# Kernel optimization log

Measured on AMD Instinct MI355X. Metric: run time of the kernel, lower is better.

## Reference

```python
import jax, jax.numpy as jnp
import numpy as np

B, L, D, H = 4, 1024, 512, 8
DH = D // H
NUM_BUCKETS = 8
MAX_DIST = 8
N_GAT_LAYERS = 2
NEG = jnp.finfo(jnp.float32).min


def _ln(x, g, b):
    m = x.mean(-1, keepdims=True)
    v = ((x - m) ** 2).mean(-1, keepdims=True)
    return (x - m) * jax.lax.rsqrt(v + 1e-5) * g + b


def _adj(parents):
    # undirected child<->parent adjacency, no self loops. parents: [B,L] int
    Bb, Ll = parents.shape
    valid = (parents >= 0) & (parents < Ll)
    p = jnp.clip(parents, 0, Ll - 1)
    bidx = jnp.arange(Bb)[:, None]
    cidx = jnp.arange(Ll)[None, :]
    A = jnp.zeros((Bb, Ll, Ll), jnp.int32).at[bidx, cidx, p].add(valid.astype(jnp.int32))
    return (A + A.transpose(0, 2, 1)) > 0


def _bucketized_dist(adj):
    # Bounded BFS: exact tree distances up to MAX_DIST; everything farther
    # lands in the same clamped bucket as distance MAX_DIST (faithful to
    # clamp(d, max=MAX_DIST) then clamp(max=NUM_BUCKETS-1) in the original).
    Bb, Ll, _ = adj.shape
    eye = jnp.eye(Ll, dtype=bool)
    Af = adj.astype(jnp.float32)
    reach = jnp.broadcast_to(eye, (Bb, Ll, Ll))
    dist = jnp.broadcast_to(jnp.where(eye, 0, MAX_DIST).astype(jnp.int32), (Bb, Ll, Ll))
    for s in range(1, MAX_DIST + 1):
        nxt = (jnp.matmul(reach.astype(jnp.float32), Af) > 0) | reach
        dist = jnp.where(nxt & ~reach, s, dist)
        reach = nxt
    return jnp.minimum(dist, NUM_BUCKETS - 1)  # bucket indices [B,L,L]


def _tree_bias(bias_table, parents, pad_mask):
    buckets = _bucketized_dist(_adj(parents))          # [B,L,L]
    bias = bias_table[:, buckets]                      # [H,B,L,L]
    bias = jnp.transpose(bias, (1, 0, 2, 3))           # [B,H,L,L]
    valid = pad_mask[:, None, None, :] & pad_mask[:, None, :, None]
    return jnp.where(valid, bias, NEG)


def _heads(z):
    Bb, Ll, _ = z.shape
    return jnp.transpose(z.reshape(Bb, Ll, H, DH), (0, 2, 1, 3))


def _attn(x, parents, pad_mask, ln1_g, ln1_b, qkv_w, qkv_b, out_w, out_b, bias_table):
    h = _ln(x, ln1_g, ln1_b)
    Bb, Ll, _ = h.shape
    qkv = (h @ qkv_w + qkv_b).reshape(Bb, Ll, 3, H, DH)
    q = jnp.transpose(qkv[:, :, 0], (0, 2, 1, 3))
    k = jnp.transpose(qkv[:, :, 1], (0, 2, 1, 3))
    v = jnp.transpose(qkv[:, :, 2], (0, 2, 1, 3))
    logits = jnp.einsum('bhid,bhjd->bhij', q, k) / np.float32(np.sqrt(DH))
    logits = logits + _tree_bias(bias_table, parents, pad_mask)
    logits = jnp.where(pad_mask[:, None, None, :], logits, NEG)
    a = jax.nn.softmax(logits, axis=-1)
    y = jnp.einsum('bhij,bhjd->bhid', a, v)
    y = jnp.transpose(y, (0, 2, 1, 3)).reshape(Bb, Ll, D)
    return y @ out_w + out_b


def _gat(x, adj_sl, pad_mask, ln_g, ln_b, wq_w, wq_b, wk_w, wk_b, wv_w, wv_b, out_w, out_b):
    h = _ln(x, ln_g, ln_b)
    Bb, Ll, _ = h.shape
    q, k, v = _heads(h @ wq_w + wq_b), _heads(h @ wk_w + wk_b), _heads(h @ wv_w + wv_b)
    logits = jnp.einsum('bhid,bhjd->bhij', q, k) / np.float32(np.sqrt(DH))
    logits = jnp.where(adj_sl[:, None], logits, NEG)
    logits = jnp.where(pad_mask[:, None, None, :], logits, NEG)
    a = jax.nn.softmax(logits, axis=-1)
    y = jnp.einsum('bhij,bhjd->bhid', a, v)
    y = jnp.transpose(y, (0, 2, 1, 3)).reshape(Bb, Ll, D)
    return x + (y @ out_w + out_b)


def _forward(x, parents, pad_mask, ln1_g, ln1_b, qkv_w, qkv_b, attn_out_w, attn_out_b,
             bias_table, gat_ln_g, gat_ln_b, gat_wq_w, gat_wq_b, gat_wk_w, gat_wk_b,
             gat_wv_w, gat_wv_b, gat_out_w, gat_out_b):
    x = x + _attn(x, parents, pad_mask, ln1_g, ln1_b, qkv_w, qkv_b,
                  attn_out_w, attn_out_b, bias_table)
    adj = _adj(parents)
    eye = jnp.eye(adj.shape[1], dtype=bool)
    adj_sl = (adj | eye) & pad_mask[:, :, None] & pad_mask[:, None, :]
    for l in range(N_GAT_LAYERS):
        x = _gat(x, adj_sl, pad_mask, gat_ln_g[l], gat_ln_b[l],
                 gat_wq_w[l], gat_wq_b[l], gat_wk_w[l], gat_wk_b[l],
                 gat_wv_w[l], gat_wv_b[l], gat_out_w[l], gat_out_b[l])
    return x


def setup_inputs() -> dict:
    key = jax.random.key(0)
    ks = jax.random.split(key, 16)
    x = jax.random.normal(ks[0], (B, L, D), jnp.float32)
    # valid random tree: parents[i] in [0, i-1], root (i=0) has parent -1
    u = jax.random.uniform(ks[1], (B, L))
    parents = jnp.floor(u * jnp.arange(L, dtype=jnp.float32)).astype(jnp.int32)
    parents = parents.at[:, 0].set(-1)
    pad_mask = jnp.ones((B, L), dtype=bool)
    w = lambda k, shp: jax.random.normal(k, shp, jnp.float32) * 0.02
    return {
        'x': x, 'parents': parents, 'pad_mask': pad_mask,
        'ln1_g': jnp.ones((D,), jnp.float32), 'ln1_b': jnp.zeros((D,), jnp.float32),
        'qkv_w': w(ks[2], (D, 3 * D)), 'qkv_b': jnp.zeros((3 * D,), jnp.float32),
        'attn_out_w': w(ks[3], (D, D)), 'attn_out_b': jnp.zeros((D,), jnp.float32),
        'bias_table': w(ks[4], (H, NUM_BUCKETS)),
        'gat_ln_g': jnp.ones((N_GAT_LAYERS, D), jnp.float32),
        'gat_ln_b': jnp.zeros((N_GAT_LAYERS, D), jnp.float32),
        'gat_wq_w': w(ks[5], (N_GAT_LAYERS, D, D)), 'gat_wq_b': jnp.zeros((N_GAT_LAYERS, D), jnp.float32),
        'gat_wk_w': w(ks[6], (N_GAT_LAYERS, D, D)), 'gat_wk_b': jnp.zeros((N_GAT_LAYERS, D), jnp.float32),
        'gat_wv_w': w(ks[7], (N_GAT_LAYERS, D, D)), 'gat_wv_b': jnp.zeros((N_GAT_LAYERS, D), jnp.float32),
        'gat_out_w': w(ks[8], (N_GAT_LAYERS, D, D)), 'gat_out_b': jnp.zeros((N_GAT_LAYERS, D), jnp.float32),
    }


def reference(x, parents, pad_mask, ln1_g, ln1_b, qkv_w, qkv_b, attn_out_w, attn_out_b,
              bias_table, gat_ln_g, gat_ln_b, gat_wq_w, gat_wq_b, gat_wk_w, gat_wk_b,
              gat_wv_w, gat_wv_b, gat_out_w, gat_out_b):
    return _forward(x, parents, pad_mask, ln1_g, ln1_b, qkv_w, qkv_b, attn_out_w,
                    attn_out_b, bias_table, gat_ln_g, gat_ln_b, gat_wq_w, gat_wq_b,
                    gat_wk_w, gat_wk_b, gat_wv_w, gat_wv_b, gat_out_w, gat_out_b)
```

## Files before the change

kernel.cpp:

```cpp
#include <hip/hip_runtime.h>
#include <hip/hip_bf16.h>
#include <math.h>

#define BB 4
#define LL 1024
#define DD 512
#define HH 8
#define DHH 64
#define MASKF -3.0e38f
#define FIXM 10.0f
#define NSPLIT 2

#define MODE_QKV 0
#define MODE_QKVR 1
#define MODE_F32C 2
#define MODE_F32S 3

typedef __attribute__((ext_vector_type(4))) float f32x4;
typedef __attribute__((ext_vector_type(8))) __bf16 bf16x8;

__device__ __forceinline__ unsigned short f2bf(float x) {
  return __builtin_bit_cast(unsigned short, __float2bfloat16(x));
}
__device__ __forceinline__ float bf2f(unsigned int u16) {
  unsigned int v = u16 << 16;
  return __builtin_bit_cast(float, v);
}
__device__ __forceinline__ float wave_sum(float v) {
#pragma unroll
  for (int o = 32; o > 0; o >>= 1) v += __shfl_xor(v, o, 64);
  return v;
}
__device__ __forceinline__ void gl16(const void* g, void* l) {
  __builtin_amdgcn_global_load_lds(
      (const __attribute__((address_space(1))) unsigned int*)g,
      (__attribute__((address_space(3))) unsigned int*)l, 16, 0, 0);
}

__global__ __launch_bounds__(256) void prep_kernel(
    const int* __restrict__ parents, const float* w0, const float* w1,
    const float* w2, const float* w3, const float* w4, const float* w5,
    const float* w6, const float* w7, const float* w8, const float* w9,
    unsigned char* __restrict__ bfr, unsigned short* __restrict__ wt) {
  __shared__ __align__(16) char psm[16640];
  const int bid = blockIdx.x;
  const int tid = threadIdx.x;
  if (bid < 1024) {
    int* si = reinterpret_cast<int*>(psm);
    int* sj = si + 576;
    const int jt = bid & 15, qt = (bid >> 4) & 15, b = bid >> 8;
    if (tid < 128) {
      const int* pp = parents + b * 1024;
      const int base = (tid < 64) ? (qt * 64 + tid) : (jt * 64 + (tid - 64));
      int* dst = (tid < 64) ? (si + tid * 9) : (sj + (tid - 64) * 9);
      int cur = base;
      dst[0] = cur;
#pragma unroll
      for (int s = 1; s <= 8; ++s) {
        int nxt = -1;
        if (cur >= 0) {
          int p = pp[cur];
          if (p >= 0 && p < 1024) nxt = p;
        }
        dst[s] = nxt;
        cur = nxt;
      }
    }
    __syncthreads();
    const int w = tid >> 6, lane = tid & 63, g = lane >> 4, lr = lane & 15;
    int ui[9];
#pragma unroll
    for (int a = 0; a < 9; ++a) ui[a] = si[(w * 16 + lr) * 9 + a];
    unsigned int dw[4];
#pragma unroll
    for (int t = 0; t < 4; ++t) {
      unsigned int d = 0;
#pragma unroll
      for (int r = 0; r < 4; ++r) {
        const int jl = t * 16 + g * 4 + r;
        int uj[9];
#pragma unroll
        for (int c = 0; c < 9; ++c) uj[c] = sj[jl * 9 + c];
        int dist = 255;
#pragma unroll
        for (int a = 0; a < 9; ++a) {
          const int va = ui[a];
          if (va >= 0) {
#pragma unroll
            for (int c = 0; c < 9; ++c)
              if (va == uj[c] && a + c < dist) dist = a + c;
          }
        }
        d |= (unsigned int)(dist < 7 ? dist : 7) << (8 * r);
      }
      dw[t] = d;
    }
    uint4 o;
    o.x = dw[0]; o.y = dw[1]; o.z = dw[2]; o.w = dw[3];
    *reinterpret_cast<uint4*>(bfr + (((size_t)b * 16 + qt) * 16 + jt) * 4096 +
                              tid * 16) = o;
  } else {
    float (*ts)[65] = reinterpret_cast<float(*)[65]>(psm);
    const int flat = bid - 1024;
    const int kx = flat & 7, ny = (flat >> 3) % 24, z = flat / 192;
    const float* src;
    int N = 512;
    size_t doff;
    switch (z) {
      case 0: src = w0; N = 1536; doff = 0; break;
      case 1: src = w1; doff = 786432; break;
      case 2: src = w2; doff = 1048576; break;
      case 3: src = w3; doff = 1048576 + 262144; break;
      case 4: src = w4; doff = 1048576 + 524288; break;
      case 5: src = w5; doff = 1835008; break;
      case 6: src = w6; doff = 2097152; break;
      case 7: src = w7; doff = 2097152 + 262144; break;
      case 8: src = w8; doff = 2097152 + 524288; break;
      default: src = w9; doff = 2883584; break;
    }
    const int n0 = ny * 64;
    if (n0 >= N) return;
    const int k0 = kx * 64;
    const int r = tid >> 4, c4 = (tid & 15) * 4;
#pragma unroll
    for (int p = 0; p < 4; ++p) {
      float4 v = *reinterpret_cast<const float4*>(src + (size_t)(k0 + p * 16 + r) * N +
                                                  n0 + c4);
      ts[p * 16 + r][c4 + 0] = v.x;
      ts[p * 16 + r][c4 + 1] = v.y;
      ts[p * 16 + r][c4 + 2] = v.z;
      ts[p * 16 + r][c4 + 3] = v.w;
    }
    __syncthreads();
#pragma unroll
    for (int p = 0; p < 4; ++p) {
      int n = p * 16 + r;
      ushort4 o;
      o.x = f2bf(ts[c4 + 0][n]);
      o.y = f2bf(ts[c4 + 1][n]);
      o.z = f2bf(ts[c4 + 2][n]);
      o.w = f2bf(ts[c4 + 3][n]);
      *reinterpret_cast<ushort4*>(wt + doff + (size_t)(n0 + n) * 512 + k0 + c4) = o;
    }
  }
}

__global__ __launch_bounds__(1024) void csr_kernel(const int* __restrict__ parents,
                                                   int* __restrict__ cptr,
                                                   int* __restrict__ cidx) {
  const int b = blockIdx.x, i = threadIdx.x;
  __shared__ int cnt[1024];
  __shared__ int wsum[16];
  const int p = parents[b * 1024 + i];
  const bool valid = (p >= 0 && p < 1024);
  cnt[i] = 0;
  __syncthreads();
  if (valid) atomicAdd(&cnt[p], 1);
  __syncthreads();
  const int v = cnt[i];
  const int lane = i & 63, wv = i >> 6;
  int s = v;
#pragma unroll
  for (int o = 1; o < 64; o <<= 1) {
    int t = __shfl_up(s, o, 64);
    if (lane >= o) s += t;
  }
  if (lane == 63) wsum[wv] = s;
  __syncthreads();
  if (wv == 0 && lane < 16) {
    int ws = wsum[lane];
#pragma unroll
    for (int o = 1; o < 16; o <<= 1) {
      int t = __shfl_up(ws, o, 64);
      if (lane >= o) ws += t;
    }
    wsum[lane] = ws;
  }
  __syncthreads();
  const int incl = s + (wv > 0 ? wsum[wv - 1] : 0);
  const int excl = incl - v;
  cptr[b * 1025 + i] = excl;
  if (i == 1023) cptr[b * 1025 + 1024] = incl;
  __syncthreads();
  cnt[i] = excl;
  __syncthreads();
  if (valid) {
    int pos = atomicAdd(&cnt[p], 1);
    cidx[b * 1024 + pos] = i;
  }
}

__global__ __launch_bounds__(256) void ln_kernel(const float* __restrict__ x,
                                                 const float* __restrict__ g,
                                                 const float* __restrict__ bta,
                                                 unsigned short* __restrict__ out) {
  const int row = blockIdx.x * 4 + (threadIdx.x >> 6);
  const int ln = threadIdx.x & 63;
  const float* xp = x + (size_t)row * DD + ln * 8;
  float4 a = *reinterpret_cast<const float4*>(xp);
  float4 c = *reinterpret_cast<const float4*>(xp + 4);
  float s = a.x + a.y + a.z + a.w + c.x + c.y + c.z + c.w;
  s = wave_sum(s);
  float mean = s * (1.f / DD);
  float dx[8] = {a.x - mean, a.y - mean, a.z - mean, a.w - mean,
                 c.x - mean, c.y - mean, c.z - mean, c.w - mean};
  float vs = 0.f;
#pragma unroll
  for (int t = 0; t < 8; ++t) vs += dx[t] * dx[t];
  vs = wave_sum(vs);
  float r = rsqrtf(vs * (1.f / DD) + 1e-5f);
  const float* gp = g + ln * 8;
  const float* bp = bta + ln * 8;
  float4 g0 = *reinterpret_cast<const float4*>(gp);
  float4 g1 = *reinterpret_cast<const float4*>(gp + 4);
  float4 b0 = *reinterpret_cast<const float4*>(bp);
  float4 b1 = *reinterpret_cast<const float4*>(bp + 4);
  float v0 = dx[0] * r * g0.x + b0.x, v1 = dx[1] * r * g0.y + b0.y;
  float v2 = dx[2] * r * g0.z + b0.z, v3 = dx[3] * r * g0.w + b0.w;
  float v4 = dx[4] * r * g1.x + b1.x, v5 = dx[5] * r * g1.y + b1.y;
  float v6 = dx[6] * r * g1.z + b1.z, v7 = dx[7] * r * g1.w + b1.w;
  uint4 pk;
  pk.x = (unsigned)f2bf(v0) | ((unsigned)f2bf(v1) << 16);
  pk.y = (unsigned)f2bf(v2) | ((unsigned)f2bf(v3) << 16);
  pk.z = (unsigned)f2bf(v4) | ((unsigned)f2bf(v5) << 16);
  pk.w = (unsigned)f2bf(v6) | ((unsigned)f2bf(v7) << 16);
  *reinterpret_cast<uint4*>(out + (size_t)row * DD + ln * 8) = pk;
}

template <int MODE>
__global__ __launch_bounds__(256) void mfma_gemm(
    const unsigned short* __restrict__ A, const unsigned short* __restrict__ A2,
    const float* __restrict__ lpart, const unsigned short* __restrict__ WT,
    const float* __restrict__ bias, const float* __restrict__ bias2,
    const float* __restrict__ bias3, const float* __restrict__ resid,
    float* __restrict__ outF, unsigned short* __restrict__ qb,
    unsigned short* __restrict__ kb, unsigned short* __restrict__ vt) {
  __shared__ __align__(16) char lds[2][8192];
  const int tid = threadIdx.x;
  const int w = tid >> 6, lane = tid & 63, g = lane >> 4, lr = lane & 15;
  const int wm = w >> 1, wn = w & 1;
  const int bm = blockIdx.y * 64, bn = blockIdx.x * 64;
  const int am = bm + w * 16 + lr;
  const f32x4 fz = {0.f, 0.f, 0.f, 0.f};
  f32x4 acc[2][2];
#pragma unroll
  for (int mi = 0; mi < 2; ++mi)
#pragma unroll
    for (int nj = 0; nj < 2; ++nj) acc[mi][nj] = fz;

  auto loadA = [&](int k0, uint4& a0, uint4& a1, float& l0, float& l1) {
    a0 = *reinterpret_cast<const uint4*>(A + (size_t)am * 512 + k0 + g * 8);
    a1 = *reinterpret_cast<const uint4*>(A2 + (size_t)am * 512 + k0 + g * 8);
    const int li = ((am >> 10) * 8 + ((k0 + g * 8) >> 6)) * 1024 + (am & 1023);
    l0 = lpart[li];
    l1 = lpart[BB * HH * LL + li];
  };
  auto writeA = [&](uint4 a0, uint4 a1, float l0, float l1, int buf) {
    const float il = 1.f / (l0 + l1);
    unsigned int o[4];
#pragma unroll
    for (int i = 0; i < 4; ++i) {
      unsigned int x0 = (&a0.x)[i], x1 = (&a1.x)[i];
      float lo = (bf2f(x0 & 0xffffu) + bf2f(x1 & 0xffffu)) * il;
      float hi = (bf2f(x0 >> 16) + bf2f(x1 >> 16)) * il;
      o[i] = (unsigned int)f2bf(lo) | ((unsigned int)f2bf(hi) << 16);
    }
    *reinterpret_cast<uint4*>(lds[buf] + w * 1024 + lane * 16) =
        make_uint4(o[0], o[1], o[2], o[3]);
  };

  if (MODE == MODE_F32C) {
    uint4 a0, a1;
    float l0, l1;
    loadA(0, a0, a1, l0, l1);
    writeA(a0, a1, l0, l1, 0);
  } else {
    gl16(A + ((size_t)am * 512 + g * 8), lds[0] + w * 1024);
  }
  gl16(WT + ((size_t)(bn + w * 16 + lr) * 512 + g * 8), lds[0] + 4096 + w * 1024);
  __syncthreads();

  uint4 a0n, a1n;
  float l0n, l1n;
  for (int ks = 0; ks < 16; ++ks) {
    const int nxt = (ks + 1) & 1;
    if (ks < 15) {
      const int k1 = (ks + 1) * 32;
      if (MODE == MODE_F32C)
        loadA(k1, a0n, a1n, l0n, l1n);
      else
        gl16(A + ((size_t)am * 512 + k1 + g * 8), lds[nxt] + w * 1024);
      gl16(WT + ((size_t)(bn + w * 16 + lr) * 512 + k1 + g * 8),
           lds[nxt] + 4096 + w * 1024);
    }
    const char* lb = lds[ks & 1];
    bf16x8 af[2], bf[2];
#pragma unroll
    for (int mi = 0; mi < 2; ++mi)
      af[mi] = *reinterpret_cast<const bf16x8*>(lb + (wm * 2 + mi) * 1024 + lane * 16);
#pragma unroll
    for (int nj = 0; nj < 2; ++nj)
      bf[nj] =
          *reinterpret_cast<const bf16x8*>(lb + 4096 + (wn * 2 + nj) * 1024 + lane * 16);
#pragma unroll
    for (int mi = 0; mi < 2; ++mi)
#pragma unroll
      for (int nj = 0; nj < 2; ++nj)
        acc[mi][nj] =
            __builtin_amdgcn_mfma_f32_16x16x32_bf16(af[mi], bf[nj], acc[mi][nj], 0, 0, 0);
    if (MODE == MODE_F32C && ks < 15) writeA(a0n, a1n, l0n, l1n, nxt);
    __syncthreads();
  }
#pragma unroll
  for (int mi = 0; mi < 2; ++mi) {
#pragma unroll
    for (int nj = 0; nj < 2; ++nj) {
#pragma unroll
      for (int r = 0; r < 4; ++r) {
        const int m = bm + wm * 32 + mi * 16 + g * 4 + r;
        const int n = bn + wn * 32 + nj * 16 + lr;
        float bv = (n < 512) ? bias[n] : (n < 1024) ? bias2[n - 512] : bias3[n - 1024];
        float v = acc[mi][nj][r] + bv;
        if (MODE == MODE_F32C || MODE == MODE_F32S) {
          outF[(size_t)m * 512 + n] = v + resid[(size_t)m * 512 + n];
        } else {
          if (n < 512)
            qb[(size_t)m * 512 + n] = f2bf(v);
          else if (n < 1024)
            kb[(size_t)m * 512 + (n - 512)] = f2bf(v);
          else {
            int nv = n - 1024;
            if (MODE == MODE_QKV)
              vt[(((size_t)(m >> 10) * 8 + (nv >> 6)) * 64 + (nv & 63)) * 1024 +
                 (m & 1023)] = f2bf(v);
            else
              vt[(size_t)m * 512 + nv] = f2bf(v);
          }
        }
      }
    }
  }
}

__global__ __launch_bounds__(256) void attn_mfma(
    const unsigned short* __restrict__ Qb, const unsigned short* __restrict__ Kb,
    const unsigned short* __restrict__ Vt, const unsigned char* __restrict__ bfr,
    const float* __restrict__ btab, unsigned short* __restrict__ Opart,
    float* __restrict__ lpart) {
  __shared__ __align__(16) char smem[28704];
  const int qt = blockIdx.x & 15, sp = blockIdx.x >> 4;
  const int h = blockIdx.y, b = blockIdx.z;
  const int q0 = qt * 64;
  const int tid = threadIdx.x;
  const int w = tid >> 6, lane = tid & 63, g = lane >> 4, lr = lane & 15;
  float* tbl = reinterpret_cast<float*>(smem + 28672);
  if (tid < 8) tbl[tid] = btab[h * 8 + tid];

  const unsigned short* qp =
      Qb + (size_t)(b * LL + q0 + w * 16 + lr) * 512 + h * 64 + g * 8;
  const bf16x8 qf0 = *reinterpret_cast<const bf16x8*>(qp);
  const bf16x8 qf1 = *reinterpret_cast<const bf16x8*>(qp + 32);

  const f32x4 fz = {0.f, 0.f, 0.f, 0.f};
  f32x4 oacc[4];
  float lsum = 0.f;
#pragma unroll
  for (int r = 0; r < 4; ++r) oacc[r] = fz;
  const int jrow = lane >> 3, jc = lane & 7;
  const size_t btbase = ((size_t)b * 16 + qt) * 16 * 4096;
  const int NT = 16 / NSPLIT;

  for (int jt = 0; jt < NT; ++jt) {
    const int ja = sp * NT + jt;
    {
      char* sb = smem;
      const int j0 = ja * 64;
#pragma unroll
      for (int ii = 0; ii < 2; ++ii) {
        const int i = w + ii * 4;
        const int j = i * 8 + jrow;
        gl16(Kb + (size_t)(b * LL + j0 + j) * 512 + h * 64 + ((jc ^ (j & 7)) * 8),
             sb + i * 1024);
        gl16(Vt + ((size_t)(b * 8 + h) * 64 + j) * 1024 + j0 + ((jc ^ (j & 7)) * 8),
             sb + 8192 + i * 1024);
      }
      gl16(bfr + btbase + (size_t)ja * 4096 + w * 1024 + lane * 16,
           sb + 16384 + w * 1024);
    }
    __syncthreads();
    const char* sb = smem;
    f32x4 s[4];
#pragma unroll
    for (int t = 0; t < 4; ++t) s[t] = fz;
#pragma unroll
    for (int t = 0; t < 4; ++t) {
#pragma unroll
      for (int kh = 0; kh < 2; ++kh) {
        bf16x8 kf = *reinterpret_cast<const bf16x8*>(
            sb + (t * 16 + lr) * 128 + (((kh * 4 + g) ^ (lr & 7)) * 16));
        s[t] = __builtin_amdgcn_mfma_f32_16x16x32_bf16(kf, kh ? qf1 : qf0, s[t], 0, 0, 0);
      }
    }
    const uint4 bq = *reinterpret_cast<const uint4*>(sb + 16384 + tid * 16);
    float pv[4][4];
#pragma unroll
    for (int t = 0; t < 4; ++t) {
      const unsigned int dw = (&bq.x)[t];
#pragma unroll
      for (int r = 0; r < 4; ++r) {
        const int bk = (dw >> (8 * r)) & 255;
        float sv = s[t][r] * 0.125f + tbl[bk];
        const float p = __expf(sv - FIXM);
        pv[t][r] = p;
        lsum += p;
      }
    }
    char* ps = smem + 20480 + w * 2048;
#pragma unroll
    for (int t = 0; t < 4; ++t) {
      unsigned int lo = (unsigned int)f2bf(pv[t][0]) | ((unsigned int)f2bf(pv[t][1]) << 16);
      unsigned int hi = (unsigned int)f2bf(pv[t][2]) | ((unsigned int)f2bf(pv[t][3]) << 16);
      *reinterpret_cast<uint2*>(ps + lr * 128 + (((2 * t + (g >> 1)) ^ (lr & 7)) * 16) +
                                (g & 1) * 8) = make_uint2(lo, hi);
    }
#pragma unroll
    for (int jh = 0; jh < 2; ++jh) {
      bf16x8 pf = *reinterpret_cast<const bf16x8*>(ps + lr * 128 +
                                                   (((jh * 4 + g) ^ (lr & 7)) * 16));
#pragma unroll
      for (int d = 0; d < 4; ++d) {
        bf16x8 vf = *reinterpret_cast<const bf16x8*>(
            sb + 8192 + (d * 16 + lr) * 128 + (((jh * 4 + g) ^ (lr & 7)) * 16));
        oacc[d] = __builtin_amdgcn_mfma_f32_16x16x32_bf16(pf, vf, oacc[d], 0, 0, 0);
      }
    }
    __syncthreads();
  }
  float ls = lsum;
  ls += __shfl_xor(ls, 16, 64);
  ls += __shfl_xor(ls, 32, 64);
  if (g == 0)
    lpart[sp * (BB * HH * LL) + (b * 8 + h) * 1024 + q0 + w * 16 + lr] = ls;
  unsigned short* Op = Opart + (size_t)sp * (BB * LL * DD);
#pragma unroll
  for (int r = 0; r < 4; ++r) {
    const int row = b * LL + q0 + w * 16 + g * 4 + r;
#pragma unroll
    for (int d = 0; d < 4; ++d)
      Op[(size_t)row * 512 + h * 64 + d * 16 + lr] = f2bf(oacc[d][r]);
  }
}

__global__ __launch_bounds__(256) void gat_attn(
    const unsigned short* __restrict__ qb, const unsigned short* __restrict__ kb,
    const unsigned short* __restrict__ vb, const int* __restrict__ parents,
    const int* __restrict__ cptr, const int* __restrict__ cidx,
    unsigned short* __restrict__ y) {
  const int b = blockIdx.y;
  const int q = blockIdx.x * 4 + (threadIdx.x >> 6);
  const int lane = threadIdx.x & 63;
  const size_t rowq = (size_t)(b * 1024 + q) * 512 + lane * 8;
  float qf[8], of[8] = {};
  {
    uint4 u = *reinterpret_cast<const uint4*>(qb + rowq);
#pragma unroll
    for (int i = 0; i < 4; ++i) {
      qf[2 * i] = bf2f((&u.x)[i] & 0xffffu);
      qf[2 * i + 1] = bf2f((&u.x)[i] >> 16);
    }
  }
  float lsum = 0.f;
  const int p = parents[b * 1024 + q];
  const int c0 = cptr[b * 1025 + q], c1 = cptr[b * 1025 + q + 1];

  auto body = [&](int j) {
    const size_t rj = (size_t)(b * 1024 + j) * 512 + lane * 8;
    uint4 ku = *reinterpret_cast<const uint4*>(kb + rj);
    float dot = 0.f;
#pragma unroll
    for (int i = 0; i < 4; ++i) {
      dot = fmaf(qf[2 * i], bf2f((&ku.x)[i] & 0xffffu), dot);
      dot = fmaf(qf[2 * i + 1], bf2f((&ku.x)[i] >> 16), dot);
    }
    dot += __shfl_xor(dot, 1, 64);
    dot += __shfl_xor(dot, 2, 64);
    dot += __shfl_xor(dot, 4, 64);
    const float pe = __expf(dot * 0.125f - FIXM);
    lsum += pe;
    uint4 vu = *reinterpret_cast<const uint4*>(vb + rj);
#pragma unroll
    for (int i = 0; i < 4; ++i) {
      of[2 * i] = fmaf(pe, bf2f((&vu.x)[i] & 0xffffu), of[2 * i]);
      of[2 * i + 1] = fmaf(pe, bf2f((&vu.x)[i] >> 16), of[2 * i + 1]);
    }
  };
  body(q);
  if (p >= 0 && p < 1024) body(p);
  for (int c = c0; c < c1; ++c) body(cidx[b * 1024 + c]);

  const float inv = 1.f / lsum;
  uint4 pk;
#pragma unroll
  for (int i = 0; i < 4; ++i)
    (&pk.x)[i] = (unsigned int)f2bf(of[2 * i] * inv) |
                 ((unsigned int)f2bf(of[2 * i + 1] * inv) << 16);
  *reinterpret_cast<uint4*>(y + rowq) = pk;
}

extern "C" void kernel_launch(void* const* d_in, const int* in_sizes, int n_in,
                              void* d_out, int out_size, void* d_ws, size_t ws_size,
                              hipStream_t stream) {
  const float* x = (const float*)d_in[0];
  const int* parents = (const int*)d_in[1];
  const float* ln1_g = (const float*)d_in[3];
  const float* ln1_b = (const float*)d_in[4];
  const float* qkv_w = (const float*)d_in[5];
  const float* qkv_b = (const float*)d_in[6];
  const float* attn_out_w = (const float*)d_in[7];
  const float* attn_out_b = (const float*)d_in[8];
  const float* bias_table = (const float*)d_in[9];
  const float* gat_ln_g = (const float*)d_in[10];
  const float* gat_ln_b = (const float*)d_in[11];
  const float* gat_wq_w = (const float*)d_in[12];
  const float* gat_wq_b = (const float*)d_in[13];
  const float* gat_wk_w = (const float*)d_in[14];
  const float* gat_wk_b = (const float*)d_in[15];
  const float* gat_wv_w = (const float*)d_in[16];
  const float* gat_wv_b = (const float*)d_in[17];
  const float* gat_out_w = (const float*)d_in[18];
  const float* gat_out_b = (const float*)d_in[19];
  float* out = (float*)d_out;

  char* wsp = (char*)d_ws;
  size_t off = 0;
  auto alloc = [&](size_t bytes) {
    void* p = wsp + off;
    off += (bytes + 255) & ~(size_t)255;
    return p;
  };
  unsigned char* bfr = (unsigned char*)alloc((size_t)BB * LL * LL);
  unsigned short* hb = (unsigned short*)alloc((size_t)BB * LL * DD * 2);
  unsigned short* qb = (unsigned short*)alloc((size_t)BB * LL * DD * 2);
  unsigned short* kb = (unsigned short*)alloc((size_t)BB * LL * DD * 2);
  unsigned short* vtb = (unsigned short*)alloc((size_t)BB * LL * DD * 2);
  unsigned short* yb = (unsigned short*)alloc((size_t)BB * LL * DD * 2);
  unsigned short* wt = (unsigned short*)alloc((size_t)3145728 * 2);
  unsigned short* Opart = (unsigned short*)alloc((size_t)NSPLIT * BB * LL * DD * 2);
  float* lpart = (float*)alloc((size_t)NSPLIT * BB * HH * LL * sizeof(float));
  int* cptr = (int*)alloc((size_t)BB * 1025 * sizeof(int));
  int* cidx = (int*)alloc((size_t)BB * LL * sizeof(int));
  (void)ws_size;

  unsigned short* O1 = Opart + (size_t)BB * LL * DD;

  prep_kernel<<<2944, 256, 0, stream>>>(parents, qkv_w, attn_out_w, gat_wq_w, gat_wk_w,
                                        gat_wv_w, gat_out_w, gat_wq_w + 262144,
                                        gat_wk_w + 262144, gat_wv_w + 262144,
                                        gat_out_w + 262144, bfr, wt);
  csr_kernel<<<4, 1024, 0, stream>>>(parents, cptr, cidx);

  ln_kernel<<<BB * LL / 4, 256, 0, stream>>>(x, ln1_g, ln1_b, hb);
  mfma_gemm<MODE_QKV><<<dim3(24, 64), 256, 0, stream>>>(
      hb, nullptr, nullptr, wt, qkv_b, qkv_b + 512, qkv_b + 1024, nullptr, nullptr, qb,
      kb, vtb);
  attn_mfma<<<dim3(16 * NSPLIT, 8, 4), 256, 0, stream>>>(qb, kb, vtb, bfr, bias_table,
                                                         Opart, lpart);
  mfma_gemm<MODE_F32C><<<dim3(8, 64), 256, 0, stream>>>(
      Opart, O1, lpart, wt + 786432, attn_out_b, nullptr, nullptr, x, out, nullptr,
      nullptr, nullptr);

  for (int l = 0; l < 2; ++l) {
    unsigned short* wfused = wt + 1048576 + (size_t)l * 1048576;
    unsigned short* wo = wfused + 786432;
    ln_kernel<<<BB * LL / 4, 256, 0, stream>>>(out, gat_ln_g + l * DD, gat_ln_b + l * DD,
                                               hb);
    mfma_gemm<MODE_QKVR><<<dim3(24, 64), 256, 0, stream>>>(
        hb, nullptr, nullptr, wfused, gat_wq_b + l * DD, gat_wk_b + l * DD,
        gat_wv_b + l * DD, nullptr, nullptr, qb, kb, vtb);
    gat_attn<<<dim3(256, 4), 256, 0, stream>>>(qb, kb, vtb, parents, cptr, cidx, yb);
    mfma_gemm<MODE_F32S><<<dim3(8, 64), 256, 0, stream>>>(
        yb, nullptr, nullptr, wo, gat_out_b + l * DD, nullptr, nullptr, out, out,
        nullptr, nullptr, nullptr);
  }
}
```

Measured before the change: 225.1 us.

## Fuse layernorm into QKV GEMMs via precomputed row stats; merge CSR into prep

Removes the separate layernorm kernels and the bf16 hb buffer. Row sum and sum-of-squares partials are now produced by an extra prep-kernel branch for the input and by the output-projection GEMM epilogues for the residual stream. The QKV GEMMs read fp32 activations, normalize them on the fly and write bf16 into LDS. The CSR build also moves into the prep kernel as extra blocks, which cuts four launches and an extra pass over activations. The cost is a heavier A-load path in the QKV GEMM (fp32 plus gamma and beta loads), extra reduction work in the epilogues, and variance computed as E[x²]−mean², which is less numerically stable.

```diff
diff --git a/kernel.cpp b/kernel.cpp
--- a/kernel.cpp
+++ b/kernel.cpp
@@ -7,9 +7,9 @@
 #define DD 512
 #define HH 8
 #define DHH 64
-#define MASKF -3.0e38f
 #define FIXM 10.0f
 #define NSPLIT 2
+#define SSTRIDE 32768
 
 #define MODE_QKV 0
 #define MODE_QKVR 1
@@ -26,11 +26,6 @@
   unsigned int v = u16 << 16;
   return __builtin_bit_cast(float, v);
 }
-__device__ __forceinline__ float wave_sum(float v) {
-#pragma unroll
-  for (int o = 32; o > 0; o >>= 1) v += __shfl_xor(v, o, 64);
-  return v;
-}
 __device__ __forceinline__ void gl16(const void* g, void* l) {
   __builtin_amdgcn_global_load_lds(
       (const __attribute__((address_space(1))) unsigned int*)g,
@@ -38,10 +33,12 @@
 }
 
 __global__ __launch_bounds__(256) void prep_kernel(
-    const int* __restrict__ parents, const float* w0, const float* w1,
-    const float* w2, const float* w3, const float* w4, const float* w5,
-    const float* w6, const float* w7, const float* w8, const float* w9,
-    unsigned char* __restrict__ bfr, unsigned short* __restrict__ wt) {
+    const int* __restrict__ parents, const float* __restrict__ xin,
+    const float* w0, const float* w1, const float* w2, const float* w3,
+    const float* w4, const float* w5, const float* w6, const float* w7,
+    const float* w8, const float* w9, unsigned char* __restrict__ bfr,
+    unsigned short* __restrict__ wt, int* __restrict__ cptr,
+    int* __restrict__ cidx, float* __restrict__ stats) {
   __shared__ __align__(16) char psm[16640];
   const int bid = blockIdx.x;
   const int tid = threadIdx.x;
@@ -99,7 +96,7 @@
     o.x = dw[0]; o.y = dw[1]; o.z = dw[2]; o.w = dw[3];
     *reinterpret_cast<uint4*>(bfr + (((size_t)b * 16 + qt) * 16 + jt) * 4096 +
                               tid * 16) = o;
-  } else {
+  } else if (bid < 2944) {
     float (*ts)[65] = reinterpret_cast<float(*)[65]>(psm);
     const int flat = bid - 1024;
     const int kx = flat & 7, ny = (flat >> 3) % 24, z = flat / 192;
@@ -142,99 +139,91 @@
       o.w = f2bf(ts[c4 + 3][n]);
       *reinterpret_cast<ushort4*>(wt + doff + (size_t)(n0 + n) * 512 + k0 + c4) = o;
     }
-  }
-}
-
-__global__ __launch_bounds__(1024) void csr_kernel(const int* __restrict__ parents,
-                                                   int* __restrict__ cptr,
-                                                   int* __restrict__ cidx) {
-  const int b = blockIdx.x, i = threadIdx.x;
-  __shared__ int cnt[1024];
-  __shared__ int wsum[16];
-  const int p = parents[b * 1024 + i];
-  const bool valid = (p >= 0 && p < 1024);
-  cnt[i] = 0;
-  __syncthreads();
-  if (valid) atomicAdd(&cnt[p], 1);
-  __syncthreads();
-  const int v = cnt[i];
-  const int lane = i & 63, wv = i >> 6;
-  int s = v;
-#pragma unroll
-  for (int o = 1; o < 64; o <<= 1) {
-    int t = __shfl_up(s, o, 64);
-    if (lane >= o) s += t;
-  }
-  if (lane == 63) wsum[wv] = s;
-  __syncthreads();
-  if (wv == 0 && lane < 16) {
-    int ws = wsum[lane];
-#pragma unroll
-    for (int o = 1; o < 16; o <<= 1) {
-      int t = __shfl_up(ws, o, 64);
-      if (lane >= o) ws += t;
-    }
-    wsum[lane] = ws;
-  }
-  __syncthreads();
-  const int incl = s + (wv > 0 ? wsum[wv - 1] : 0);
-  const int excl = incl - v;
-  cptr[b * 1025 + i] = excl;
-  if (i == 1023) cptr[b * 1025 + 1024] = incl;
-  __syncthreads();
-  cnt[i] = excl;
-  __syncthreads();
-  if (valid) {
-    int pos = atomicAdd(&cnt[p], 1);
-    cidx[b * 1024 + pos] = i;
-  }
-}
-
-__global__ __launch_bounds__(256) void ln_kernel(const float* __restrict__ x,
-                                                 const float* __restrict__ g,
-                                                 const float* __restrict__ bta,
-                                                 unsigned short* __restrict__ out) {
-  const int row = blockIdx.x * 4 + (threadIdx.x >> 6);
-  const int ln = threadIdx.x & 63;
-  const float* xp = x + (size_t)row * DD + ln * 8;
-  float4 a = *reinterpret_cast<const float4*>(xp);
-  float4 c = *reinterpret_cast<const float4*>(xp + 4);
-  float s = a.x + a.y + a.z + a.w + c.x + c.y + c.z + c.w;
-  s = wave_sum(s);
-  float mean = s * (1.f / DD);
-  float dx[8] = {a.x - mean, a.y - mean, a.z - mean, a.w - mean,
-                 c.x - mean, c.y - mean, c.z - mean, c.w - mean};
-  float vs = 0.f;
-#pragma unroll
-  for (int t = 0; t < 8; ++t) vs += dx[t] * dx[t];
-  vs = wave_sum(vs);
-  float r = rsqrtf(vs * (1.f / DD) + 1e-5f);
-  const float* gp = g + ln * 8;
-  const float* bp = bta + ln * 8;
-  float4 g0 = *reinterpret_cast<const float4*>(gp);
-  float4 g1 = *reinterpret_cast<const float4*>(gp + 4);
-  float4 b0 = *reinterpret_cast<const float4*>(bp);
-  float4 b1 = *reinterpret_cast<const float4*>(bp + 4);
-  float v0 = dx[0] * r * g0.x + b0.x, v1 = dx[1] * r * g0.y + b0.y;
-  float v2 = dx[2] * r * g0.z + b0.z, v3 = dx[3] * r * g0.w + b0.w;
-  float v4 = dx[4] * r * g1.x + b1.x, v5 = dx[5] * r * g1.y + b1.y;
-  float v6 = dx[6] * r * g1.z + b1.z, v7 = dx[7] * r * g1.w + b1.w;
-  uint4 pk;
-  pk.x = (unsigned)f2bf(v0) | ((unsigned)f2bf(v1) << 16);
-  pk.y = (unsigned)f2bf(v2) | ((unsigned)f2bf(v3) << 16);
-  pk.z = (unsigned)f2bf(v4) | ((unsigned)f2bf(v5) << 16);
-  pk.w = (unsigned)f2bf(v6) | ((unsigned)f2bf(v7) << 16);
-  *reinterpret_cast<uint4*>(out + (size_t)row * DD + ln * 8) = pk;
-}
-
-template <int MODE>
+  } else if (bid < 2948) {
+    int* cnt = reinterpret_cast<int*>(psm);
+    int* excl = cnt + 1024;
+    int* wsums = excl + 1024;
+    const int b = bid - 2944;
+    const int* pp = parents + b * 1024;
+    const int lane = tid & 63, wv = tid >> 6;
+#pragma unroll
+    for (int k = 0; k < 4; ++k) cnt[tid + k * 256] = 0;
+    __syncthreads();
+    int pv[4];
+#pragma unroll
+    for (int k = 0; k < 4; ++k) pv[k] = pp[tid * 4 + k];
+#pragma unroll
+    for (int k = 0; k < 4; ++k)
+      if (pv[k] >= 0 && pv[k] < 1024) atomicAdd(&cnt[pv[k]], 1);
+    __syncthreads();
+    int c[4];
+    int cs = 0;
+#pragma unroll
+    for (int k = 0; k < 4; ++k) {
+      c[k] = cnt[tid * 4 + k];
+      cs += c[k];
+    }
+    int s = cs;
+#pragma unroll
+    for (int o = 1; o < 64; o <<= 1) {
+      int t = __shfl_up(s, o, 64);
+      if (lane >= o) s += t;
+    }
+    if (lane == 63) wsums[wv] = s;
+    __syncthreads();
+    int woff = 0;
+    for (int k = 0; k < 4; ++k)
+      if (k < wv) woff += wsums[k];
+    int e = woff + s - cs;
+#pragma unroll
+    for (int k = 0; k < 4; ++k) {
+      cptr[b * 1025 + tid * 4 + k] = e;
+      excl[tid * 4 + k] = e;
+      e += c[k];
+    }
+    if (tid == 255) cptr[b * 1025 + 1024] = woff + s;
+    __syncthreads();
+#pragma unroll
+    for (int k = 0; k < 4; ++k) {
+      const int p = pv[k];
+      if (p >= 0 && p < 1024) {
+        int pos = atomicAdd(&excl[p], 1);
+        cidx[b * 1024 + pos] = tid * 4 + k;
+      }
+    }
+  } else {
+    const int row = (bid - 2948) * 4 + (tid >> 6);
+    const int lane = tid & 63;
+    const float* xp = xin + (size_t)row * 512 + lane * 8;
+    float4 a = *reinterpret_cast<const float4*>(xp);
+    float4 c2 = *reinterpret_cast<const float4*>(xp + 4);
+    float s = a.x + a.y + a.z + a.w + c2.x + c2.y + c2.z + c2.w;
+    float q = a.x * a.x + a.y * a.y + a.z * a.z + a.w * a.w + c2.x * c2.x +
+              c2.y * c2.y + c2.z * c2.z + c2.w * c2.w;
+    s += __shfl_xor(s, 1, 64);
+    s += __shfl_xor(s, 2, 64);
+    s += __shfl_xor(s, 4, 64);
+    q += __shfl_xor(q, 1, 64);
+    q += __shfl_xor(q, 2, 64);
+    q += __shfl_xor(q, 4, 64);
+    if ((lane & 7) == 0) {
+      stats[row * 8 + (lane >> 3)] = s;
+      stats[SSTRIDE + row * 8 + (lane >> 3)] = q;
+    }
+  }
+}
+
+template <int MODE, int STATS>
 __global__ __launch_bounds__(256) void mfma_gemm(
     const unsigned short* __restrict__ A, const unsigned short* __restrict__ A2,
-    const float* __restrict__ lpart, const unsigned short* __restrict__ WT,
-    const float* __restrict__ bias, const float* __restrict__ bias2,
-    const float* __restrict__ bias3, const float* __restrict__ resid,
-    float* __restrict__ outF, unsigned short* __restrict__ qb,
-    unsigned short* __restrict__ kb, unsigned short* __restrict__ vt) {
+    const float* __restrict__ lpart, const float* __restrict__ Af,
+    const float* __restrict__ statsr, float* __restrict__ statsw,
+    const float* __restrict__ lng, const float* __restrict__ lnb,
+    const unsigned short* __restrict__ WT, const float* __restrict__ bias,
+    const float* __restrict__ bias2, const float* __restrict__ bias3,
+    const float* __restrict__ resid, float* __restrict__ outF,
+    unsigned short* __restrict__ qb, unsigned short* __restrict__ kb,
+    unsigned short* __restrict__ vt) {
   __shared__ __align__(16) char lds[2][8192];
   const int tid = threadIdx.x;
   const int w = tid >> 6, lane = tid & 63, g = lane >> 4, lr = lane & 15;
@@ -248,14 +237,26 @@
 #pragma unroll
     for (int nj = 0; nj < 2; ++nj) acc[mi][nj] = fz;
 
-  auto loadA = [&](int k0, uint4& a0, uint4& a1, float& l0, float& l1) {
+  float mean = 0.f, rstd = 0.f;
+  if (MODE == MODE_QKV || MODE == MODE_QKVR) {
+    const float4 s0 = *reinterpret_cast<const float4*>(statsr + am * 8);
+    const float4 s1 = *reinterpret_cast<const float4*>(statsr + am * 8 + 4);
+    const float4 q0 = *reinterpret_cast<const float4*>(statsr + SSTRIDE + am * 8);
+    const float4 q1 = *reinterpret_cast<const float4*>(statsr + SSTRIDE + am * 8 + 4);
+    const float sum = s0.x + s0.y + s0.z + s0.w + s1.x + s1.y + s1.z + s1.w;
+    const float sq = q0.x + q0.y + q0.z + q0.w + q1.x + q1.y + q1.z + q1.w;
+    mean = sum * (1.f / 512);
+    rstd = rsqrtf(sq * (1.f / 512) - mean * mean + 1e-5f);
+  }
+
+  auto loadC = [&](int k0, uint4& a0, uint4& a1, float& l0, float& l1) {
     a0 = *reinterpret_cast<const uint4*>(A + (size_t)am * 512 + k0 + g * 8);
     a1 = *reinterpret_cast<const uint4*>(A2 + (size_t)am * 512 + k0 + g * 8);
     const int li = ((am >> 10) * 8 + ((k0 + g * 8) >> 6)) * 1024 + (am & 1023);
     l0 = lpart[li];
     l1 = lpart[BB * HH * LL + li];
   };
-  auto writeA = [&](uint4 a0, uint4 a1, float l0, float l1, int buf) {
+  auto writeC = [&](uint4 a0, uint4 a1, float l0, float l1, int buf) {
     const float il = 1.f / (l0 + l1);
     unsigned int o[4];
 #pragma unroll
@@ -268,26 +269,56 @@
     *reinterpret_cast<uint4*>(lds[buf] + w * 1024 + lane * 16) =
         make_uint4(o[0], o[1], o[2], o[3]);
   };
+  auto loadL = [&](int k0, float4& x0, float4& x1, float4& g0, float4& g1,
+                   float4& b0, float4& b1) {
+    const float* ap = Af + (size_t)am * 512 + k0 + g * 8;
+    x0 = *reinterpret_cast<const float4*>(ap);
+    x1 = *reinterpret_cast<const float4*>(ap + 4);
+    g0 = *reinterpret_cast<const float4*>(lng + k0 + g * 8);
+    g1 = *reinterpret_cast<const float4*>(lng + k0 + g * 8 + 4);
+    b0 = *reinterpret_cast<const float4*>(lnb + k0 + g * 8);
+    b1 = *reinterpret_cast<const float4*>(lnb + k0 + g * 8 + 4);
+  };
+  auto writeL = [&](float4 x0, float4 x1, float4 g0, float4 g1, float4 b0,
+                    float4 b1, int buf) {
+    float v[8] = {(x0.x - mean) * rstd * g0.x + b0.x, (x0.y - mean) * rstd * g0.y + b0.y,
+                  (x0.z - mean) * rstd * g0.z + b0.z, (x0.w - mean) * rstd * g0.w + b0.w,
+                  (x1.x - mean) * rstd * g1.x + b1.x, (x1.y - mean) * rstd * g1.y + b1.y,
+                  (x1.z - mean) * rstd * g1.z + b1.z, (x1.w - mean) * rstd * g1.w + b1.w};
+    unsigned int o[4];
+#pragma unroll
+    for (int i = 0; i < 4; ++i)
+      o[i] = (unsigned int)f2bf(v[2 * i]) | ((unsigned int)f2bf(v[2 * i + 1]) << 16);
+    *reinterpret_cast<uint4*>(lds[buf] + w * 1024 + lane * 16) =
+        make_uint4(o[0], o[1], o[2], o[3]);
+  };
 
   if (MODE == MODE_F32C) {
     uint4 a0, a1;
     float l0, l1;
-    loadA(0, a0, a1, l0, l1);
-    writeA(a0, a1, l0, l1, 0);
+    loadC(0, a0, a1, l0, l1);
+    writeC(a0, a1, l0, l1, 0);
+  } else if (MODE == MODE_QKV || MODE == MODE_QKVR) {
+    float4 x0, x1, g0, g1, b0, b1;
+    loadL(0, x0, x1, g0, g1, b0, b1);
+    writeL(x0, x1, g0, g1, b0, b1, 0);
   } else {
     gl16(A + ((size_t)am * 512 + g * 8), lds[0] + w * 1024);
   }
   gl16(WT + ((size_t)(bn + w * 16 + lr) * 512 + g * 8), lds[0] + 4096 + w * 1024);
   __syncthreads();
 
-  uint4 a0n, a1n;
-  float l0n, l1n;
+  uint4 ca0, ca1;
+  float cl0, cl1;
+  float4 lx0, lx1, lg0, lg1, lb0, lb1;
   for (int ks = 0; ks < 16; ++ks) {
     const int nxt = (ks + 1) & 1;
     if (ks < 15) {
       const int k1 = (ks + 1) * 32;
       if (MODE == MODE_F32C)
-        loadA(k1, a0n, a1n, l0n, l1n);
+        loadC(k1, ca0, ca1, cl0, cl1);
+      else if (MODE == MODE_QKV || MODE == MODE_QKVR)
+        loadL(k1, lx0, lx1, lg0, lg1, lb0, lb1);
       else
         gl16(A + ((size_t)am * 512 + k1 + g * 8), lds[nxt] + w * 1024);
       gl16(WT + ((size_t)(bn + w * 16 + lr) * 512 + k1 + g * 8),
@@ -308,9 +339,15 @@
       for (int nj = 0; nj < 2; ++nj)
         acc[mi][nj] =
             __builtin_amdgcn_mfma_f32_16x16x32_bf16(af[mi], bf[nj], acc[mi][nj], 0, 0, 0);
-    if (MODE == MODE_F32C && ks < 15) writeA(a0n, a1n, l0n, l1n, nxt);
-    __syncthreads();
-  }
+    if (ks < 15) {
+      if (MODE == MODE_F32C)
+        writeC(ca0, ca1, cl0, cl1, nxt);
+      else if (MODE == MODE_QKV || MODE == MODE_QKVR)
+        writeL(lx0, lx1, lg0, lg1, lb0, lb1, nxt);
+    }
+    __syncthreads();
+  }
+  float ps[2][4] = {}, pq[2][4] = {};
 #pragma unroll
   for (int mi = 0; mi < 2; ++mi) {
 #pragma unroll
@@ -322,7 +359,12 @@
         float bv = (n < 512) ? bias[n] : (n < 1024) ? bias2[n - 512] : bias3[n - 1024];
         float v = acc[mi][nj][r] + bv;
         if (MODE == MODE_F32C || MODE == MODE_F32S) {
-          outF[(size_t)m * 512 + n] = v + resid[(size_t)m * 512 + n];
+          const float ov = v + resid[(size_t)m * 512 + n];
+          outF[(size_t)m * 512 + n] = ov;
+          if (STATS) {
+            ps[mi][r] += ov;
+            pq[mi][r] += ov * ov;
+          }
         } else {
           if (n < 512)
             qb[(size_t)m * 512 + n] = f2bf(v);
@@ -338,6 +380,29 @@
           }
         }
       }
+    }
+  }
+  if (STATS && (MODE == MODE_F32C || MODE == MODE_F32S)) {
+    __syncthreads();
+    float* lsum = reinterpret_cast<float*>(lds);
+    float* lsq = lsum + 2048;
+#pragma unroll
+    for (int mi = 0; mi < 2; ++mi)
+#pragma unroll
+      for (int r = 0; r < 4; ++r) {
+        const int ml = wm * 32 + mi * 16 + g * 4 + r;
+        lsum[ml * 32 + wn * 16 + lr] = ps[mi][r];
+        lsq[ml * 32 + wn * 16 + lr] = pq[mi][r];
+      }
+    __syncthreads();
+    if (tid < 64) {
+      float s = 0.f, q = 0.f;
+      for (int k = 0; k < 32; ++k) {
+        s += lsum[tid * 32 + k];
+        q += lsq[tid * 32 + k];
+      }
+      statsw[(bm + tid) * 8 + blockIdx.x] = s;
+      statsw[SSTRIDE + (bm + tid) * 8 + blockIdx.x] = q;
     }
   }
 }
@@ -539,7 +604,6 @@
     return p;
   };
   unsigned char* bfr = (unsigned char*)alloc((size_t)BB * LL * LL);
-  unsigned short* hb = (unsigned short*)alloc((size_t)BB * LL * DD * 2);
   unsigned short* qb = (unsigned short*)alloc((size_t)BB * LL * DD * 2);
   unsigned short* kb = (unsigned short*)alloc((size_t)BB * LL * DD * 2);
   unsigned short* vtb = (unsigned short*)alloc((size_t)BB * LL * DD * 2);
@@ -549,37 +613,43 @@
   float* lpart = (float*)alloc((size_t)NSPLIT * BB * HH * LL * sizeof(float));
   int* cptr = (int*)alloc((size_t)BB * 1025 * sizeof(int));
   int* cidx = (int*)alloc((size_t)BB * LL * sizeof(int));
+  float* statsX = (float*)alloc((size_t)2 * SSTRIDE * sizeof(float));
+  float* statsO = (float*)alloc((size_t)2 * SSTRIDE * sizeof(float));
   (void)ws_size;
 
   unsigned short* O1 = Opart + (size_t)BB * LL * DD;
 
-  prep_kernel<<<2944, 256, 0, stream>>>(parents, qkv_w, attn_out_w, gat_wq_w, gat_wk_w,
-                                        gat_wv_w, gat_out_w, gat_wq_w + 262144,
-                                        gat_wk_w + 262144, gat_wv_w + 262144,
-                                        gat_out_w + 262144, bfr, wt);
-  csr_kernel<<<4, 1024, 0, stream>>>(parents, cptr, cidx);
-
-  ln_kernel<<<BB * LL / 4, 256, 0, stream>>>(x, ln1_g, ln1_b, hb);
-  mfma_gemm<MODE_QKV><<<dim3(24, 64), 256, 0, stream>>>(
-      hb, nullptr, nullptr, wt, qkv_b, qkv_b + 512, qkv_b + 1024, nullptr, nullptr, qb,
-      kb, vtb);
+  prep_kernel<<<3972, 256, 0, stream>>>(parents, x, qkv_w, attn_out_w, gat_wq_w,
+                                        gat_wk_w, gat_wv_w, gat_out_w,
+                                        gat_wq_w + 262144, gat_wk_w + 262144,
+                                        gat_wv_w + 262144, gat_out_w + 262144, bfr, wt,
+                                        cptr, cidx, statsX);
+
+  mfma_gemm<MODE_QKV, 0><<<dim3(24, 64), 256, 0, stream>>>(
+      nullptr, nullptr, nullptr, x, statsX, nullptr, ln1_g, ln1_b, wt, qkv_b,
+      qkv_b + 512, qkv_b + 1024, nullptr, nullptr, qb, kb, vtb);
   attn_mfma<<<dim3(16 * NSPLIT, 8, 4), 256, 0, stream>>>(qb, kb, vtb, bfr, bias_table,
                                                          Opart, lpart);
-  mfma_gemm<MODE_F32C><<<dim3(8, 64), 256, 0, stream>>>(
-      Opart, O1, lpart, wt + 786432, attn_out_b, nullptr, nullptr, x, out, nullptr,
-      nullptr, nullptr);
+  mfma_gemm<MODE_F32C, 1><<<dim3(8, 64), 256, 0, stream>>>(
+      Opart, O1, lpart, nullptr, nullptr, statsO, nullptr, nullptr, wt + 786432,
+      attn_out_b, nullptr, nullptr, x, out, nullptr, nullptr, nullptr);
 
   for (int l = 0; l < 2; ++l) {
     unsigned short* wfused = wt + 1048576 + (size_t)l * 1048576;
     unsigned short* wo = wfused + 786432;
-    ln_kernel<<<BB * LL / 4, 256, 0, stream>>>(out, gat_ln_g + l * DD, gat_ln_b + l * DD,
-                                               hb);
-    mfma_gemm<MODE_QKVR><<<dim3(24, 64), 256, 0, stream>>>(
-        hb, nullptr, nullptr, wfused, gat_wq_b + l * DD, gat_wk_b + l * DD,
+    mfma_gemm<MODE_QKVR, 0><<<dim3(24, 64), 256, 0, stream>>>(
+        nullptr, nullptr, nullptr, out, statsO, nullptr, gat_ln_g + l * DD,
+        gat_ln_b + l * DD, wfused, gat_wq_b + l * DD, gat_wk_b + l * DD,
         gat_wv_b + l * DD, nullptr, nullptr, qb, kb, vtb);
     gat_attn<<<dim3(256, 4), 256, 0, stream>>>(qb, kb, vtb, parents, cptr, cidx, yb);
-    mfma_gemm<MODE_F32S><<<dim3(8, 64), 256, 0, stream>>>(
-        yb, nullptr, nullptr, wo, gat_out_b + l * DD, nullptr, nullptr, out, out,
-        nullptr, nullptr, nullptr);
-  }
-}
+    if (l == 0) {
+      mfma_gemm<MODE_F32S, 1><<<dim3(8, 64), 256, 0, stream>>>(
+          yb, nullptr, nullptr, nullptr, nullptr, statsO, nullptr, nullptr, wo,
+          gat_out_b, nullptr, nullptr, out, out, nullptr, nullptr, nullptr);
+    } else {
+      mfma_gemm<MODE_F32S, 0><<<dim3(8, 64), 256, 0, stream>>>(
+          yb, nullptr, nullptr, nullptr, nullptr, nullptr, nullptr, nullptr, wo,
+          gat_out_b + DD, nullptr, nullptr, out, out, nullptr, nullptr, nullptr);
+    }
+  }
+}
```

Result: slower. 282.0 us (+25.3%).
